# Optimization experiments

Hardware: AMD Instinct MI355X
Metric: run time of the kernel (lower is better)

The kernel has to match this reference:

```python
import jax, jax.numpy as jnp
import numpy as np

B, P, C, H, W = 4, 500000, 32, 512, 512
INT_MAX = np.iinfo(np.int32).max


def setup_inputs() -> dict:
    key = jax.random.key(0)
    k1, k2, k3, k4 = jax.random.split(key, 4)
    point_features = jax.random.normal(k1, (C, B * P), dtype=jnp.float32)
    default_features = jax.random.normal(k2, (C, 1), dtype=jnp.float32)
    # points in a frustum in front of an identity camera: z in [1,10], x/y spread with depth
    z = jax.random.uniform(k3, (B * P,), minval=1.0, maxval=10.0)
    xy = jax.random.uniform(k4, (B * P, 2), minval=-1.0, maxval=1.0) * (0.4 * z)[:, None]
    point_clouds = jnp.concatenate([xy, z[:, None]], axis=1).astype(jnp.float32)
    K = jnp.array([[500.0, 0.0, W / 2.0], [0.0, 500.0, H / 2.0], [0.0, 0.0, 1.0]], jnp.float32)
    cam_intrinsic = jnp.tile(K[None], (B, 1, 1))
    E = jnp.concatenate([jnp.eye(3, dtype=jnp.float32), jnp.zeros((3, 1), jnp.float32)], axis=1)
    cam_extrinsic = jnp.tile(E[None], (B, 1, 1))
    near_far_max_splatting_size = jnp.tile(jnp.array([0.1, 100.0, 1.0], jnp.float32)[None], (B, 1))
    num_points = jnp.full((B,), P, dtype=jnp.int32)
    return dict(point_features=point_features, default_features=default_features,
                point_clouds=point_clouds, cam_intrinsic=cam_intrinsic,
                cam_extrinsic=cam_extrinsic,
                near_far_max_splatting_size=near_far_max_splatting_size,
                num_points=num_points, tar_height=H, tar_width=W)


def _rasterize_one(pts, K, E, nf, Hh, Ww):
    # pts: [P,3]. E columns are camera X/Y/Z axes and camera center T
    # (PCPR reorders them to [Z,X,Y,T] before calling the CUDA kernel).
    Xax, Yax, Zax, T = E[:, 0], E[:, 1], E[:, 2], E[:, 3]
    d = pts - T                       # [P,3]
    zc = d @ Zax                      # depth along camera Z
    zs = jnp.where(zc == 0, 1.0, zc)  # avoid div-by-zero; such points are culled anyway
    u = K[0, 0] * (d @ Xax) / zs + K[0, 2]
    v = K[1, 1] * (d @ Yax) / zs + K[1, 2]
    ui = jnp.floor(u).astype(jnp.int32)
    vi = jnp.floor(v).astype(jnp.int32)
    valid = (zc > nf[0]) & (zc < nf[1]) & (ui >= 0) & (ui < Ww) & (vi >= 0) & (vi < Hh)
    pix = jnp.where(valid, vi * Ww + ui, 0)
    npix = Hh * Ww
    inf = jnp.float32(jnp.inf)
    dmin = jnp.full((npix,), inf, jnp.float32).at[pix].min(jnp.where(valid, zc, inf))
    win = valid & (zc == dmin[pix])
    pid = jnp.arange(pts.shape[0], dtype=jnp.int32)
    idx = jnp.full((npix,), INT_MAX, dtype=jnp.int32).at[pix].min(jnp.where(win, pid, INT_MAX))
    empty = idx == INT_MAX
    idx = jnp.where(empty, pts.shape[0], idx)  # empty pixel -> default-feature column
    depth = jnp.where(empty, jnp.float32(0.0), dmin)
    return idx.reshape(Hh, Ww), depth.reshape(Hh, Ww)


def reference(point_features, default_features, point_clouds, cam_intrinsic,
              cam_extrinsic, near_far_max_splatting_size, num_points,
              tar_height, tar_width):
    Bn = cam_intrinsic.shape[0]
    Cd = point_features.shape[0]
    Pn = point_clouds.shape[0] // Bn  # equal point count per batch item
    pts = point_clouds.reshape(Bn, Pn, 3)
    rast = jax.vmap(lambda p, k, e, nf: _rasterize_one(p, k, e, nf, tar_height, tar_width))
    idx, depth = rast(pts, cam_intrinsic, cam_extrinsic[:, 0:3, 0:4], near_far_max_splatting_size)
    # per-batch feature table [C, P+D]; empty pixels hit column P (default features)
    pf = point_features.reshape(Cd, Bn, Pn).transpose(1, 0, 2)  # [B,C,P]
    dflt = jnp.broadcast_to(default_features[None], (Bn, Cd, default_features.shape[1]))
    feats = jnp.concatenate([pf, dflt], axis=2)                 # [B,C,P+D]
    gather = jax.vmap(lambda f, ix: jnp.take(f, ix.reshape(-1), axis=1)
                      .reshape(f.shape[0], tar_height, tar_width))
    out_feature = gather(feats, idx)          # [B,C,H,W]
    out_depth = depth[:, None]                # [B,1,H,W]
    return out_feature, out_depth
```

## Files before the change

kernel.cpp:

```cpp
#include <hip/hip_runtime.h>
#include <cstdint>
#include <cstddef>

#define TH 256

typedef float vfloat4 __attribute__((ext_vector_type(4)));

__device__ __forceinline__ unsigned int f32_to_bf16_rne(float x) {
    const unsigned int u = __float_as_uint(x);
    return (u + 0x7FFFu + ((u >> 16) & 1u)) >> 16;
}
__device__ __forceinline__ float bf16_bits_to_f32(unsigned int h) {
    return __uint_as_float(h << 16);
}

__global__ void init_packed_kernel(ulonglong2* __restrict__ packed, int n2)
{
    const int i = blockIdx.x * blockDim.x + threadIdx.x;
    if (i < n2) packed[i] = make_ulonglong2(~0ull, ~0ull);
}

__device__ __forceinline__ bool project_point(
    const float* __restrict__ pc, const float* __restrict__ K,
    const float* __restrict__ E, const float* __restrict__ nf,
    int b, int p, int P, int Hh, int Ww,
    int& pix_out, float& zc_out)
{
    const int i = b * P + p;
    const float x = pc[3 * i + 0];
    const float y = pc[3 * i + 1];
    const float z = pc[3 * i + 2];
    const float* Eb = E + b * 12;
    const float dx = x - Eb[3], dy = y - Eb[7], dz = z - Eb[11];
    const float zc = dx * Eb[2] + dy * Eb[6] + dz * Eb[10];
    const float zs = (zc == 0.0f) ? 1.0f : zc;
    const float* Kb = K + b * 9;
    const float u = Kb[0] * (dx * Eb[0] + dy * Eb[4] + dz * Eb[8]) / zs + Kb[2];
    const float v = Kb[4] * (dx * Eb[1] + dy * Eb[5] + dz * Eb[9]) / zs + Kb[5];
    const int ui = (int)floorf(u);
    const int vi = (int)floorf(v);
    const float nf0 = nf[b * 3 + 0], nf1 = nf[b * 3 + 1];
    const bool valid = (zc > nf0) && (zc < nf1) &&
                       (ui >= 0) && (ui < Ww) && (vi >= 0) && (vi < Hh);
    pix_out = vi * Ww + ui;
    zc_out  = zc;
    return valid;
}

__global__ void fused_raster_transpose_kernel(
    const float* __restrict__ pc, const float* __restrict__ K,
    const float* __restrict__ E, const float* __restrict__ nf,
    const float* __restrict__ feats,
    unsigned long long* __restrict__ packed,
    uint4* __restrict__ tfeat,
    int P, int npix, int Hh, int Ww, int Bn)
{
    __shared__ unsigned int lds[32 * 129];
    const int b = blockIdx.y;
    const int t = threadIdx.x;
    const int p0 = blockIdx.x * 256;
    if (p0 >= P) return;
    const size_t BP = (size_t)Bn * P;
    const size_t gbase = (size_t)b * P + p0;

    bool valid = false;
    int pix = 0; float zc = 0.0f;
    {
        const int p = p0 + t;
        if (p < P) valid = project_point(pc, K, E, nf, b, p, P, Hh, Ww, pix, zc);
    }

    const int tn = P - p0;
    if (tn >= 256) {
        #pragma unroll
        for (int k = 0; k < 8; ++k) {
            const int i = t + k * 256;
            const int c = i >> 6, col4 = i & 63;
            const vfloat4 v = __builtin_nontemporal_load(
                (const vfloat4*)(feats + (size_t)c * BP + gbase + (size_t)col4 * 4));
            const unsigned int w0 = f32_to_bf16_rne(v.x) | (f32_to_bf16_rne(v.y) << 16);
            const unsigned int w1 = f32_to_bf16_rne(v.z) | (f32_to_bf16_rne(v.w) << 16);
            lds[c * 129 + 2 * col4]     = w0;
            lds[c * 129 + 2 * col4 + 1] = w1;
        }
        __syncthreads();
        #pragma unroll
        for (int k = 0; k < 4; ++k) {
            const int o = t + k * 256;
            const int pl = o >> 2, q = o & 3;
            const int wsel = pl >> 1;
            const int hsel = (pl & 1) * 16;
            unsigned int wd[4];
            #pragma unroll
            for (int m = 0; m < 4; ++m) {
                const int c0 = 8 * q + 2 * m;
                const unsigned int a  = lds[c0 * 129 + wsel];
                const unsigned int bb = lds[(c0 + 1) * 129 + wsel];
                wd[m] = ((a >> hsel) & 0xFFFFu) | (((bb >> hsel) & 0xFFFFu) << 16);
            }
            tfeat[gbase * 4 + o] = make_uint4(wd[0], wd[1], wd[2], wd[3]);
        }
    } else {
        if (t < tn) {
            const size_t p = gbase + t;
            #pragma unroll
            for (int grp = 0; grp < 4; ++grp) {
                unsigned int wd[4];
                #pragma unroll
                for (int kk = 0; kk < 4; ++kk) {
                    const int c0 = grp * 8 + 2 * kk;
                    wd[kk] = f32_to_bf16_rne(feats[(size_t)c0 * BP + p]) |
                             (f32_to_bf16_rne(feats[(size_t)(c0 + 1) * BP + p]) << 16);
                }
                tfeat[p * 4 + grp] = make_uint4(wd[0], wd[1], wd[2], wd[3]);
            }
        }
    }

    if (valid) {
        const unsigned long long pk =
            ((unsigned long long)__float_as_uint(zc) << 32) |
            (unsigned int)(p0 + t);
        atomicMin(&packed[(size_t)b * npix + pix], pk);
    }
}

__global__ void gather_output_kernel(
    const unsigned long long* __restrict__ packed,
    const uint4* __restrict__ tfeat,
    const float* __restrict__ dflt,
    float* __restrict__ out_feat,
    float* __restrict__ out_depth,
    int P, int npix)
{
    const int b = blockIdx.y;
    const int pix = blockIdx.x * blockDim.x + threadIdx.x;
    if (pix >= npix) return;

    const size_t gi = (size_t)b * npix + pix;
    const unsigned long long pk = packed[gi];
    const bool empty = (pk == ~0ull);

    __builtin_nontemporal_store(
        empty ? 0.0f : __uint_as_float((unsigned int)(pk >> 32)),
        out_depth + gi);

    float f[32];
    if (empty) {
        #pragma unroll
        for (int c = 0; c < 32; ++c) f[c] = dflt[c];
    } else {
        const unsigned int pid = (unsigned int)(pk & 0xFFFFFFFFull);
        const uint4* src = tfeat + ((size_t)b * P + pid) * 4;
        #pragma unroll
        for (int q = 0; q < 4; ++q) {
            const uint4 v = src[q];
            const unsigned int ws[4] = {v.x, v.y, v.z, v.w};
            #pragma unroll
            for (int k = 0; k < 4; ++k) {
                f[q * 8 + 2 * k]     = bf16_bits_to_f32(ws[k] & 0xFFFFu);
                f[q * 8 + 2 * k + 1] = bf16_bits_to_f32(ws[k] >> 16);
            }
        }
    }

    float* of = out_feat + ((size_t)b * 32) * npix + pix;
    #pragma unroll
    for (int c = 0; c < 32; ++c)
        __builtin_nontemporal_store(f[c], of + (size_t)c * npix);
}

__global__ void rasterize_fb_kernel(
    const float* __restrict__ pc, const float* __restrict__ K,
    const float* __restrict__ E, const float* __restrict__ nf,
    unsigned long long* __restrict__ packed,
    int P, int Hh, int Ww)
{
    const int b = blockIdx.y;
    const int p = blockIdx.x * blockDim.x + threadIdx.x;
    if (p >= P) return;
    int pix; float zc;
    if (!project_point(pc, K, E, nf, b, p, P, Hh, Ww, pix, zc)) return;
    const unsigned long long pk =
        ((unsigned long long)__float_as_uint(zc) << 32) | (unsigned int)p;
    atomicMin(&packed[(size_t)b * Hh * Ww + pix], pk);
}

__global__ void scatter_kernel(
    const float* __restrict__ pc, const float* __restrict__ K,
    const float* __restrict__ E, const float* __restrict__ nf,
    const unsigned long long* __restrict__ packed,
    const float* __restrict__ feats,
    float* __restrict__ out_feat,
    int B, int P, int C, int Hh, int Ww)
{
    const int b = blockIdx.y;
    const int p = blockIdx.x * blockDim.x + threadIdx.x;
    if (p >= P) return;
    int pix; float zc;
    if (!project_point(pc, K, E, nf, b, p, P, Hh, Ww, pix, zc)) return;
    const int npix = Hh * Ww;
    const unsigned long long pk = packed[(size_t)b * npix + pix];
    if ((unsigned int)(pk & 0xFFFFFFFFull) != (unsigned int)p) return;
    const size_t stride = (size_t)B * P;
    const size_t src0   = (size_t)b * P + p;
    float* of = out_feat + ((size_t)b * C) * npix + pix;
    for (int c = 0; c < C; ++c) of[(size_t)c * npix] = feats[(size_t)c * stride + src0];
}

__global__ void finalize_kernel(
    const unsigned long long* __restrict__ packed,
    const float* __restrict__ dflt,
    float* __restrict__ out_feat, float* __restrict__ out_depth,
    int C, int npix)
{
    const int b = blockIdx.y;
    const int pix = blockIdx.x * blockDim.x + threadIdx.x;
    if (pix >= npix) return;
    const size_t gi = (size_t)b * npix + pix;
    const unsigned long long pk = packed[gi];
    const bool empty = (pk == ~0ull);
    out_depth[gi] = empty ? 0.0f : __uint_as_float((unsigned int)(pk >> 32));
    if (empty) {
        float* of = out_feat + ((size_t)b * C) * npix + pix;
        for (int c = 0; c < C; ++c) of[(size_t)c * npix] = dflt[c];
    }
}

extern "C" void kernel_launch(void* const* d_in, const int* in_sizes, int n_in,
                              void* d_out, int out_size, void* d_ws, size_t ws_size,
                              hipStream_t stream) {
    const float* point_features = (const float*)d_in[0];
    const float* default_feats  = (const float*)d_in[1];
    const float* point_clouds   = (const float*)d_in[2];
    const float* cam_K          = (const float*)d_in[3];
    const float* cam_E          = (const float*)d_in[4];
    const float* near_far       = (const float*)d_in[5];

    const int B  = in_sizes[3] / 9;
    const int BP = in_sizes[2] / 3;
    const int P  = BP / B;
    const int C  = in_sizes[0] / BP;
    const int Hh = 512, Ww = 512;
    const int npix = Hh * Ww;

    unsigned long long* packed = (unsigned long long*)d_ws;
    uint4* tfeat = (uint4*)((char*)d_ws + (size_t)B * npix * 8);

    const size_t need = (size_t)B * npix * 8 + (size_t)BP * 64;

    float* out_feat  = (float*)d_out;
    float* out_depth = (float*)d_out + (size_t)B * C * npix;

    const dim3 blk(TH);
    const dim3 grid_pts((P + TH - 1) / TH, B);
    const dim3 grid_pix((npix + TH - 1) / TH, B);

    const int n2 = (B * npix) / 2;
    init_packed_kernel<<<(n2 + TH - 1) / TH, blk, 0, stream>>>(
        (ulonglong2*)packed, n2);

    if (ws_size >= need && C == 32) {
        fused_raster_transpose_kernel<<<grid_pts, blk, 0, stream>>>(
            point_clouds, cam_K, cam_E, near_far, point_features,
            packed, tfeat, P, npix, Hh, Ww, B);
        gather_output_kernel<<<grid_pix, blk, 0, stream>>>(
            packed, tfeat, default_feats, out_feat, out_depth, P, npix);
    } else {
        rasterize_fb_kernel<<<grid_pts, blk, 0, stream>>>(
            point_clouds, cam_K, cam_E, near_far, packed, P, Hh, Ww);
        finalize_kernel<<<grid_pix, blk, 0, stream>>>(
            packed, default_feats, out_feat, out_depth, C, npix);
        scatter_kernel<<<grid_pts, blk, 0, stream>>>(
            point_clouds, cam_K, cam_E, near_far, packed, point_features,
            out_feat, B, P, C, Hh, Ww);
    }
}
```

Baseline: 139.9 us.

## Split 64-bit z-buffer atomic into 32-bit depth min plus resolve pass

Replaces the single 64-bit packed atomicMin (depth|index) with a 32-bit atomicMin on depth, stores each point's pixel and depth to a buffer, and adds a resolve kernel that does a 32-bit atomicMin on index for points matching the winning depth. The aim is to avoid the cost of 64-bit atomics. In exchange it adds an extra kernel launch, an extra pass over 2M points, and 8 bytes per point of workspace traffic.

```diff
diff --git a/kernel.cpp b/kernel.cpp
--- a/kernel.cpp
+++ b/kernel.cpp
@@ -6,6 +6,9 @@
 
 typedef float vfloat4 __attribute__((ext_vector_type(4)));
 
+#define PIX_INVALID 0xFFFFFFFFu
+#define IDX_EMPTY   0x7FFFFFFFu
+
 __device__ __forceinline__ unsigned int f32_to_bf16_rne(float x) {
     const unsigned int u = __float_as_uint(x);
     return (u + 0x7FFFu + ((u >> 16) & 1u)) >> 16;
@@ -14,10 +17,14 @@
     return __uint_as_float(h << 16);
 }
 
-__global__ void init_packed_kernel(ulonglong2* __restrict__ packed, int n2)
+__global__ void init_zbuf_kernel(uint4* __restrict__ dmin4,
+                                 uint4* __restrict__ idx4, int n4)
 {
     const int i = blockIdx.x * blockDim.x + threadIdx.x;
-    if (i < n2) packed[i] = make_ulonglong2(~0ull, ~0ull);
+    if (i < n4) {
+        dmin4[i] = make_uint4(PIX_INVALID, PIX_INVALID, PIX_INVALID, PIX_INVALID);
+        idx4[i]  = make_uint4(IDX_EMPTY, IDX_EMPTY, IDX_EMPTY, IDX_EMPTY);
+    }
 }
 
 __device__ __forceinline__ bool project_point(
@@ -51,7 +58,8 @@
     const float* __restrict__ pc, const float* __restrict__ K,
     const float* __restrict__ E, const float* __restrict__ nf,
     const float* __restrict__ feats,
-    unsigned long long* __restrict__ packed,
+    unsigned int* __restrict__ dmin,
+    uint2* __restrict__ pix_buf,
     uint4* __restrict__ tfeat,
     int P, int npix, int Hh, int Ww, int Bn)
 {
@@ -67,7 +75,11 @@
     int pix = 0; float zc = 0.0f;
     {
         const int p = p0 + t;
-        if (p < P) valid = project_point(pc, K, E, nf, b, p, P, Hh, Ww, pix, zc);
+        if (p < P) {
+            valid = project_point(pc, K, E, nf, b, p, P, Hh, Ww, pix, zc);
+            pix_buf[gbase + t] = make_uint2(valid ? (unsigned int)pix : PIX_INVALID,
+                                            __float_as_uint(zc));
+        }
     }
 
     const int tn = P - p0;
@@ -118,15 +130,30 @@
     }
 
     if (valid) {
-        const unsigned long long pk =
-            ((unsigned long long)__float_as_uint(zc) << 32) |
-            (unsigned int)(p0 + t);
-        atomicMin(&packed[(size_t)b * npix + pix], pk);
+        atomicMin(&dmin[(size_t)b * npix + pix], __float_as_uint(zc));
+    }
+}
+
+__global__ void resolve_kernel(
+    const uint2* __restrict__ pix_buf,
+    const unsigned int* __restrict__ dmin,
+    unsigned int* __restrict__ idx,
+    int P, int npix)
+{
+    const int b = blockIdx.y;
+    const int p = blockIdx.x * blockDim.x + threadIdx.x;
+    if (p >= P) return;
+
+    const uint2 pr = pix_buf[(size_t)b * P + p];
+    if (pr.x == PIX_INVALID) return;
+    if (dmin[(size_t)b * npix + pr.x] == pr.y) {
+        atomicMin(&idx[(size_t)b * npix + pr.x], (unsigned int)p);
     }
 }
 
 __global__ void gather_output_kernel(
-    const unsigned long long* __restrict__ packed,
+    const unsigned int* __restrict__ dmin,
+    const unsigned int* __restrict__ idx,
     const uint4* __restrict__ tfeat,
     const float* __restrict__ dflt,
     float* __restrict__ out_feat,
@@ -138,20 +165,18 @@
     if (pix >= npix) return;
 
     const size_t gi = (size_t)b * npix + pix;
-    const unsigned long long pk = packed[gi];
-    const bool empty = (pk == ~0ull);
+    const unsigned int ix = idx[gi];
+    const bool empty = (ix == IDX_EMPTY);
 
     __builtin_nontemporal_store(
-        empty ? 0.0f : __uint_as_float((unsigned int)(pk >> 32)),
-        out_depth + gi);
+        empty ? 0.0f : __uint_as_float(dmin[gi]), out_depth + gi);
 
     float f[32];
     if (empty) {
         #pragma unroll
         for (int c = 0; c < 32; ++c) f[c] = dflt[c];
     } else {
-        const unsigned int pid = (unsigned int)(pk & 0xFFFFFFFFull);
-        const uint4* src = tfeat + ((size_t)b * P + pid) * 4;
+        const uint4* src = tfeat + ((size_t)b * P + ix) * 4;
         #pragma unroll
         for (int q = 0; q < 4; ++q) {
             const uint4 v = src[q];
@@ -168,6 +193,12 @@
     #pragma unroll
     for (int c = 0; c < 32; ++c)
         __builtin_nontemporal_store(f[c], of + (size_t)c * npix);
+}
+
+__global__ void init_packed_kernel(ulonglong2* __restrict__ packed, int n2)
+{
+    const int i = blockIdx.x * blockDim.x + threadIdx.x;
+    if (i < n2) packed[i] = make_ulonglong2(~0ull, ~0ull);
 }
 
 __global__ void rasterize_fb_kernel(
@@ -244,10 +275,12 @@
     const int Hh = 512, Ww = 512;
     const int npix = Hh * Ww;
 
-    unsigned long long* packed = (unsigned long long*)d_ws;
-    uint4* tfeat = (uint4*)((char*)d_ws + (size_t)B * npix * 8);
-
-    const size_t need = (size_t)B * npix * 8 + (size_t)BP * 64;
+    unsigned int* dmin = (unsigned int*)d_ws;
+    unsigned int* idx  = dmin + (size_t)B * npix;
+    uint2* pix_buf = (uint2*)((char*)d_ws + (size_t)B * npix * 8);
+    uint4* tfeat = (uint4*)((char*)d_ws + (size_t)B * npix * 8 + (size_t)BP * 8);
+
+    const size_t need = (size_t)B * npix * 8 + (size_t)BP * 8 + (size_t)BP * 64;
 
     float* out_feat  = (float*)d_out;
     float* out_depth = (float*)d_out + (size_t)B * C * npix;
@@ -256,17 +289,22 @@
     const dim3 grid_pts((P + TH - 1) / TH, B);
     const dim3 grid_pix((npix + TH - 1) / TH, B);
 
-    const int n2 = (B * npix) / 2;
-    init_packed_kernel<<<(n2 + TH - 1) / TH, blk, 0, stream>>>(
-        (ulonglong2*)packed, n2);
-
     if (ws_size >= need && C == 32) {
+        const int n4 = (B * npix) / 4;
+        init_zbuf_kernel<<<(n4 + TH - 1) / TH, blk, 0, stream>>>(
+            (uint4*)dmin, (uint4*)idx, n4);
         fused_raster_transpose_kernel<<<grid_pts, blk, 0, stream>>>(
             point_clouds, cam_K, cam_E, near_far, point_features,
-            packed, tfeat, P, npix, Hh, Ww, B);
+            dmin, pix_buf, tfeat, P, npix, Hh, Ww, B);
+        resolve_kernel<<<grid_pts, blk, 0, stream>>>(
+            pix_buf, dmin, idx, P, npix);
         gather_output_kernel<<<grid_pix, blk, 0, stream>>>(
-            packed, tfeat, default_feats, out_feat, out_depth, P, npix);
+            dmin, idx, tfeat, default_feats, out_feat, out_depth, P, npix);
     } else {
+        unsigned long long* packed = (unsigned long long*)d_ws;
+        const int n2 = (B * npix) / 2;
+        init_packed_kernel<<<(n2 + TH - 1) / TH, blk, 0, stream>>>(
+            (ulonglong2*)packed, n2);
         rasterize_fb_kernel<<<grid_pts, blk, 0, stream>>>(
             point_clouds, cam_K, cam_E, near_far, packed, P, Hh, Ww);
         finalize_kernel<<<grid_pix, blk, 0, stream>>>(
```

Result: slower. 171.2 us (+22.3%).
